# Performance work log

Measured on AMD Instinct MI355X. Metric: run time of the kernel, lower is better.

## Reference

```python
import jax, jax.numpy as jnp
from jax import lax
import numpy as np

D_MODEL = 768
D_STATE = 64
D_CONV = 4
EXPAND = 2
HEADDIM = 128
NGROUPS = 1
D_INNER = EXPAND * D_MODEL            # 1536
NHEADS = D_INNER // HEADDIM           # 12
D_IN_PROJ = 2 * D_INNER + 2 * NGROUPS * D_STATE + NHEADS  # 3212
CONV_DIM = D_INNER + 2 * NGROUPS * D_STATE                # 1664
BATCH, SEQLEN = 2, 4096
EPS = 1e-5


def setup_inputs() -> dict:
    key = jax.random.key(0)
    ks = jax.random.split(key, 8)
    u = jax.random.normal(ks[0], (BATCH, SEQLEN, D_MODEL), jnp.float32)
    W_in = jax.random.normal(ks[1], (D_IN_PROJ, D_MODEL), jnp.float32) * 0.02
    conv_w = jax.random.normal(ks[2], (CONV_DIM, D_CONV), jnp.float32) * 0.2
    conv_b = jnp.zeros((CONV_DIM,), jnp.float32)
    # dt_bias init as in BaseMambaBlock: inv-softplus of dt ~ logU(dt_min, dt_max)
    dt = jnp.exp(jax.random.uniform(ks[3], (NHEADS,)) * (np.log(0.1) - np.log(0.001)) + np.log(0.001))
    dt = jnp.clip(dt, 1e-4, None)
    dt_bias = dt + jnp.log(-jnp.expm1(-dt))
    A_log = jnp.log(jnp.abs(jax.random.normal(ks[4], (NHEADS,), jnp.float32)))
    Dp = jnp.ones((NHEADS,), jnp.float32)
    norm_w = jnp.ones((D_INNER,), jnp.float32)
    W_out = jax.random.normal(ks[5], (D_MODEL, D_INNER), jnp.float32) * 0.02
    return dict(u=u, W_in=W_in, conv_w=conv_w, conv_b=conv_b, dt_bias=dt_bias,
                A_log=A_log, Dp=Dp, norm_w=norm_w, W_out=W_out)


def _silu(x):
    return x * jax.nn.sigmoid(x)


def _depthwise_causal_conv(x, w, b):
    # x: [B, L, C], w: [C, W], b: [C]. Causal: left-pad W-1, crop to L.
    Bt, L, C = x.shape
    xp = jnp.pad(x, ((0, 0), (D_CONV - 1, 0), (0, 0)))
    # stack D_CONV shifted views: [B, L, C, W]
    taps = jnp.stack([xp[:, k:k + L, :] for k in range(D_CONV)], axis=-1)
    return jnp.einsum('blcw,cw->blc', taps, w) + b


def reference(u, W_in, conv_w, conv_b, dt_bias, A_log, Dp, norm_w, W_out):
    Bt, L, _ = u.shape
    zxbcdt = jnp.einsum('bld,ed->ble', u, W_in)  # [B, L, 3212]
    z = zxbcdt[..., :D_INNER]                                   # [B,L,1536]
    xBC = zxbcdt[..., D_INNER:D_INNER + CONV_DIM]               # [B,L,1664]
    dt = zxbcdt[..., D_INNER + CONV_DIM:]                       # [B,L,H]
    dt = jax.nn.softplus(dt + dt_bias)                          # [B,L,H]

    xBC = _silu(_depthwise_causal_conv(xBC, conv_w, conv_b))
    x = xBC[..., :D_INNER].reshape(Bt, L, NHEADS, HEADDIM)      # [B,L,H,P]
    Bm = xBC[..., D_INNER:D_INNER + NGROUPS * D_STATE]          # [B,L,N] (ngroups=1)
    Cm = xBC[..., D_INNER + NGROUPS * D_STATE:]                 # [B,L,N]

    A = -jnp.exp(A_log)                                         # [H]
    dA = jnp.exp(dt * A)                                        # [B,L,H]

    # time-major scan over the selective-state-space recurrence
    xs = (jnp.swapaxes(x, 0, 1),   # [L,B,H,P]
          jnp.swapaxes(dt, 0, 1),  # [L,B,H]
          jnp.swapaxes(dA, 0, 1),  # [L,B,H]
          jnp.swapaxes(Bm, 0, 1),  # [L,B,N]
          jnp.swapaxes(Cm, 0, 1))  # [L,B,N]

    def step(state, inp):
        x_t, dt_t, dA_t, B_t, C_t = inp
        # state: [B,H,P,N]
        state = state * dA_t[..., None, None] + (dt_t[..., None] * x_t)[..., None] * B_t[:, None, None, :]
        y_t = jnp.einsum('bhpn,bn->bhp', state, C_t)
        return state, y_t

    state0 = jnp.zeros((Bt, NHEADS, HEADDIM, D_STATE), u.dtype)
    _, y = lax.scan(step, state0, xs)                           # y: [L,B,H,P]
    y = jnp.swapaxes(y, 0, 1) + Dp[None, None, :, None] * x     # skip term D*x
    y = y.reshape(Bt, L, D_INNER)

    # RMSNormGated, norm_before_gate=False: normalize(y * silu(z)) * weight
    g = y * _silu(z)
    g = g * jax.lax.rsqrt(jnp.mean(g * g, axis=-1, keepdims=True) + EPS) * norm_w
    return jnp.einsum('bli,di->bld', g, W_out)
```

## Files before the change

kernel.cpp:

```cpp
#include <hip/hip_runtime.h>
#include <hip/hip_bf16.h>
#include <stdint.h>

#define BATCH   2
#define SEQLEN  4096
#define DMODEL  768
#define DSTATE  64
#define DCONV   4
#define HEADDIM 128
#define NHEADS  12
#define DINNER  1536
#define DINPROJ 3212
#define CONVDIM 1664
#define DXBC    1676
#define NPAD1   3328
#define ROWS    (BATCH*SEQLEN)
#define CHUNK   64
#define NCHUNK  (SEQLEN/CHUNK)
#define CROWS   8

typedef __bf16 bf16x8 __attribute__((ext_vector_type(8)));
typedef float  f32x4  __attribute__((ext_vector_type(4)));

__device__ __forceinline__ f32x4 splat4(float v) { return (f32x4){v, v, v, v}; }

__device__ __forceinline__ void load_lds16(const void* g, void* l) {
    __builtin_amdgcn_global_load_lds(
        (const __attribute__((address_space(1))) unsigned int*)g,
        (__attribute__((address_space(3))) unsigned int*)l, 16, 0, 0);
}

__global__ void cvt_bf16_kernel(const float* __restrict__ src,
                                __hip_bfloat16* __restrict__ dst, int n) {
    int i = (blockIdx.x * blockDim.x + threadIdx.x) * 4;
    if (i + 3 < n) {
        float4 v = *(const float4*)(src + i);
        dst[i + 0] = __float2bfloat16(v.x);
        dst[i + 1] = __float2bfloat16(v.y);
        dst[i + 2] = __float2bfloat16(v.z);
        dst[i + 3] = __float2bfloat16(v.w);
    } else {
        for (; i < n; ++i) dst[i] = __float2bfloat16(src[i]);
    }
}

__global__ void padw1_kernel(const float* __restrict__ src,
                             __hip_bfloat16* __restrict__ dst) {
    int i = blockIdx.x * blockDim.x + threadIdx.x;
    if (i >= NPAD1 * DMODEL) return;
    int r = i / DMODEL;
    float v = (r < DINPROJ) ? src[i] : 0.f;
    dst[i] = __float2bfloat16(v);
}

__global__ __launch_bounds__(256) void gemm_bf16_nt(
    const __hip_bfloat16* __restrict__ A,
    const __hip_bfloat16* __restrict__ Bt,
    float* __restrict__ C,
    int M, int Nreal, int K, int ldc)
{
    __shared__ __align__(16) __hip_bfloat16 As[128 * 32];
    __shared__ __align__(16) __hip_bfloat16 Bs[128 * 32];
    const int tid  = threadIdx.x;
    const int lane = tid & 63;
    const int wave = tid >> 6;
    const int wm   = wave >> 1;
    const int wn   = wave & 1;
    const int tm   = blockIdx.x * 128;
    const int tn   = blockIdx.y * 128;

    f32x4 acc[4][4] = {};

    const int lrow = tid >> 2;
    const int lk8  = (tid & 3) * 8;
    const __hip_bfloat16* gA0 = A  + (size_t)(tm + lrow)      * K + lk8;
    const __hip_bfloat16* gA1 = A  + (size_t)(tm + lrow + 64) * K + lk8;
    const __hip_bfloat16* gB0 = Bt + (size_t)(tn + lrow)      * K + lk8;
    const __hip_bfloat16* gB1 = Bt + (size_t)(tn + lrow + 64) * K + lk8;
    __hip_bfloat16* sA0 = As + tid * 8;
    __hip_bfloat16* sA1 = As + tid * 8 + 2048;
    __hip_bfloat16* sB0 = Bs + tid * 8;
    __hip_bfloat16* sB1 = Bs + tid * 8 + 2048;

    const int fr = lane & 15;
    const int fk = (lane >> 4) * 8;

    for (int kk = 0; kk < K; kk += 32) {
        load_lds16(gA0 + kk, sA0);
        load_lds16(gA1 + kk, sA1);
        load_lds16(gB0 + kk, sB0);
        load_lds16(gB1 + kk, sB1);
        __syncthreads();
        bf16x8 af[4], bfr[4];
#pragma unroll
        for (int i = 0; i < 4; ++i) {
            af[i]  = *(const bf16x8*)(As + (wm * 64 + i * 16 + fr) * 32 + fk);
            bfr[i] = *(const bf16x8*)(Bs + (wn * 64 + i * 16 + fr) * 32 + fk);
        }
#pragma unroll
        for (int mi = 0; mi < 4; ++mi)
#pragma unroll
            for (int ni = 0; ni < 4; ++ni)
                acc[mi][ni] = __builtin_amdgcn_mfma_f32_16x16x32_bf16(
                    af[mi], bfr[ni], acc[mi][ni], 0, 0, 0);
        __syncthreads();
    }

    const int rq = (lane >> 4) * 4;
#pragma unroll
    for (int mi = 0; mi < 4; ++mi) {
#pragma unroll
        for (int ni = 0; ni < 4; ++ni) {
            int col = tn + wn * 64 + ni * 16 + fr;
            if (col < Nreal) {
                size_t rbase = (size_t)(tm + wm * 64 + mi * 16 + rq) * ldc + col;
#pragma unroll
                for (int j = 0; j < 4; ++j)
                    C[rbase + (size_t)j * ldc] = acc[mi][ni][j];
            }
        }
    }
}

__global__ void conv_kernel(const float* __restrict__ xbcdt,
                            const float* __restrict__ convw,
                            const float* __restrict__ convb,
                            float* __restrict__ xbuf,
                            float* __restrict__ Bm,
                            float* __restrict__ Cm)
{
    int c = blockIdx.x * 256 + threadIdx.x;
    if (c >= CONVDIM) return;
    size_t row0 = (size_t)blockIdx.y * CROWS;
    int l0 = (int)(row0 & (SEQLEN - 1));
    float w0 = convw[c * 4 + 0];
    float w1 = convw[c * 4 + 1];
    float w2 = convw[c * 4 + 2];
    float w3 = convw[c * 4 + 3];
    float bias = convb[c];
    const float* src = xbcdt + row0 * DXBC + c;
    float x0 = (l0 >= 3) ? src[-3 * DXBC] : 0.f;
    float x1 = (l0 >= 2) ? src[-2 * DXBC] : 0.f;
    float x2 = (l0 >= 1) ? src[-1 * DXBC] : 0.f;
#pragma unroll
    for (int r = 0; r < CROWS; ++r) {
        float x3 = src[(size_t)r * DXBC];
        float acc = bias + x0 * w0 + x1 * w1 + x2 * w2 + x3 * w3;
        float v = acc / (1.f + __expf(-acc));
        size_t row = row0 + r;
        if (c < DINNER)               xbuf[row * DINNER + c] = v;
        else if (c < DINNER + DSTATE) Bm[row * DSTATE + (c - DINNER)] = v;
        else                          Cm[row * DSTATE + (c - DINNER - DSTATE)] = v;
        x0 = x1; x1 = x2; x2 = x3;
    }
}

__global__ void dt_kernel(const float* __restrict__ xbcdt,
                          const float* __restrict__ dt_bias,
                          const float* __restrict__ A_log,
                          float* __restrict__ dtb, float* __restrict__ dAb)
{
    int i = blockIdx.x * 256 + threadIdx.x;
    if (i >= ROWS * NHEADS) return;
    int row = i / NHEADS, h = i - row * NHEADS;
    float v = xbcdt[(size_t)row * DXBC + CONVDIM + h] + dt_bias[h];
    float dt = (v > 20.f) ? v : log1pf(__expf(v));
    float A = -__expf(A_log[h]);
    dtb[i] = dt;
    dAb[i] = __expf(dt * A);
}

__global__ __launch_bounds__(256) void chunk_state_f32(
    const float* __restrict__ xbuf, const float* __restrict__ Bm,
    const float* __restrict__ dtb, const float* __restrict__ dAb,
    float* __restrict__ Sloc, float* __restrict__ Pk)
{
    const int blk = blockIdx.x;
    const int k   = blk % NCHUNK;
    const int bh  = blk / NCHUNK;
    const int h   = bh % NHEADS;
    const int b   = bh / NHEADS;
    const int tid = threadIdx.x;
    const int pg  = tid >> 3;
    const int n0  = (tid & 7) * 8;
    const size_t row0 = (size_t)b * SEQLEN + k * CHUNK;
    const float* xbase = xbuf + (row0 * NHEADS + h) * HEADDIM + pg * 4;

    __shared__ __align__(16) float lB[CHUNK][DSTATE];
    __shared__ float lDA[CHUNK];
    __shared__ float ldt[CHUNK];

    for (int i = tid; i < CHUNK * DSTATE / 4; i += 256)
        ((float4*)&lB[0][0])[i] = ((const float4*)(Bm + row0 * DSTATE))[i];
    if (tid < CHUNK) {
        lDA[tid] = dAb[(row0 + tid) * NHEADS + h];
        ldt[tid] = dtb[(row0 + tid) * NHEADS + h];
    }
    __syncthreads();

    f32x4 s4[4][2] = {};
    f32x4 xt0[4], xt1[4];

#pragma unroll
    for (int tt = 0; tt < 4; ++tt)
        xt0[tt] = *(const f32x4*)(xbase + (size_t)tt * (NHEADS * HEADDIM));

#pragma unroll
    for (int tile = 0; tile < 16; ++tile) {
        f32x4* cur = (tile & 1) ? xt1 : xt0;
        f32x4* nxt = (tile & 1) ? xt0 : xt1;
        if (tile < 15) {
#pragma unroll
            for (int tt = 0; tt < 4; ++tt)
                nxt[tt] = *(const f32x4*)(xbase +
                    (size_t)((tile + 1) * 4 + tt) * (NHEADS * HEADDIM));
        }
#pragma unroll
        for (int tt = 0; tt < 4; ++tt) {
            int t = tile * 4 + tt;
            f32x4 da4 = splat4(lDA[t]);
            float dtv = ldt[t];
            f32x4 bv0 = *(const f32x4*)&lB[t][n0];
            f32x4 bv1 = *(const f32x4*)&lB[t][n0 + 4];
#pragma unroll
            for (int pl = 0; pl < 4; ++pl) {
                f32x4 dtx = splat4(dtv * cur[tt][pl]);
                s4[pl][0] = s4[pl][0] * da4 + dtx * bv0;
                s4[pl][1] = s4[pl][1] * da4 + dtx * bv1;
            }
        }
    }

    const size_t kbase = (size_t)(bh * NCHUNK + k) * (HEADDIM * DSTATE);
#pragma unroll
    for (int pl = 0; pl < 4; ++pl) {
        size_t a = kbase + (size_t)(pg * 4 + pl) * DSTATE + n0;
        *(f32x4*)(Sloc + a)     = s4[pl][0];
        *(f32x4*)(Sloc + a + 4) = s4[pl][1];
    }

    if (tid == 0) {
        float pr = 1.f;
#pragma unroll 8
        for (int t = 0; t < CHUNK; ++t) pr *= lDA[t];
        Pk[bh * NCHUNK + k] = pr;
    }
}

__global__ __launch_bounds__(256) void scan_phase2(
    float* __restrict__ Sloc, const float* __restrict__ Pk)
{
    int bh = blockIdx.x >> 5;
    int eo = (blockIdx.x & 31) * 256 + threadIdx.x;
    __shared__ float lP[NCHUNK];
    if (threadIdx.x < NCHUNK) lP[threadIdx.x] = Pk[bh * NCHUNK + threadIdx.x];
    __syncthreads();
    float s = 0.f;
    size_t base = (size_t)bh * NCHUNK * 8192 + eo;
#pragma unroll 8
    for (int k = 0; k < NCHUNK; ++k) {
        size_t a = base + (size_t)k * 8192;
        float f = Sloc[a];
        Sloc[a] = s;
        s = s * lP[k] + f;
    }
}

__global__ __launch_bounds__(256) void chunk_y_f32(
    const float* __restrict__ xbuf, const float* __restrict__ Bm,
    const float* __restrict__ Cm, const float* __restrict__ dtb,
    const float* __restrict__ dAb, const float* __restrict__ Dp,
    const float* __restrict__ Sini, float* __restrict__ ybuf)
{
    const int blk = blockIdx.x;
    const int k   = blk % NCHUNK;
    const int bh  = blk / NCHUNK;
    const int h   = bh % NHEADS;
    const int b   = bh / NHEADS;
    const int tid = threadIdx.x;
    const int pg  = tid >> 2;
    const int q   = tid & 3;
    const int n0  = q * 16;
    const size_t row0 = (size_t)b * SEQLEN + k * CHUNK;
    const float* xbase = xbuf + (row0 * NHEADS + h) * HEADDIM + pg * 2;
    float* ybase = ybuf + (row0 * NHEADS + h) * HEADDIM + pg * 2;

    __shared__ __align__(16) float lB[CHUNK][DSTATE];
    __shared__ __align__(16) float lC[CHUNK][DSTATE];
    __shared__ float lDA[CHUNK];
    __shared__ float ldt[CHUNK];

    for (int i = tid; i < CHUNK * DSTATE / 4; i += 256) {
        ((float4*)&lB[0][0])[i] = ((const float4*)(Bm + row0 * DSTATE))[i];
        ((float4*)&lC[0][0])[i] = ((const float4*)(Cm + row0 * DSTATE))[i];
    }
    if (tid < CHUNK) {
        lDA[tid] = dAb[(row0 + tid) * NHEADS + h];
        ldt[tid] = dtb[(row0 + tid) * NHEADS + h];
    }

    f32x4 s4[2][4];
    const size_t kbase = (size_t)(bh * NCHUNK + k) * (HEADDIM * DSTATE);
#pragma unroll
    for (int pl = 0; pl < 2; ++pl) {
        size_t a = kbase + (size_t)(pg * 2 + pl) * DSTATE + n0;
#pragma unroll
        for (int nq = 0; nq < 4; ++nq)
            s4[pl][nq] = *(const f32x4*)(Sini + a + nq * 4);
    }
    const float dph = Dp[h];

    float xa[2][8], xb[2][8];
#pragma unroll
    for (int tt = 0; tt < 8; ++tt) {
        float2 v = *(const float2*)(xbase + (size_t)tt * (NHEADS * HEADDIM));
        xa[0][tt] = v.x; xa[1][tt] = v.y;
    }
    __syncthreads();

#pragma unroll
    for (int tile = 0; tile < 8; ++tile) {
        float (*cur)[8] = (tile & 1) ? xb : xa;
        float (*nxt)[8] = (tile & 1) ? xa : xb;
        if (tile < 7) {
#pragma unroll
            for (int tt = 0; tt < 8; ++tt) {
                float2 v = *(const float2*)(xbase +
                    (size_t)((tile + 1) * 8 + tt) * (NHEADS * HEADDIM));
                nxt[0][tt] = v.x; nxt[1][tt] = v.y;
            }
        }
#pragma unroll
        for (int tt = 0; tt < 8; ++tt) {
            int t = tile * 8 + tt;
            f32x4 da4 = splat4(lDA[t]);
            float dtv = ldt[t];
            f32x4 bv0 = *(const f32x4*)&lB[t][n0];
            f32x4 bv1 = *(const f32x4*)&lB[t][n0 + 4];
            f32x4 bv2 = *(const f32x4*)&lB[t][n0 + 8];
            f32x4 bv3 = *(const f32x4*)&lB[t][n0 + 12];
            f32x4 cv0 = *(const f32x4*)&lC[t][n0];
            f32x4 cv1 = *(const f32x4*)&lC[t][n0 + 4];
            f32x4 cv2 = *(const f32x4*)&lC[t][n0 + 8];
            f32x4 cv3 = *(const f32x4*)&lC[t][n0 + 12];
            float yr[2];
#pragma unroll
            for (int pl = 0; pl < 2; ++pl) {
                f32x4 dtx = splat4(dtv * cur[pl][tt]);
                f32x4 v0 = s4[pl][0] * da4 + dtx * bv0;
                f32x4 v1 = s4[pl][1] * da4 + dtx * bv1;
                f32x4 v2 = s4[pl][2] * da4 + dtx * bv2;
                f32x4 v3 = s4[pl][3] * da4 + dtx * bv3;
                s4[pl][0] = v0; s4[pl][1] = v1; s4[pl][2] = v2; s4[pl][3] = v3;
                f32x4 y4 = cv0 * v0 + cv1 * v1 + cv2 * v2 + cv3 * v3;
                float y = (y4[0] + y4[1]) + (y4[2] + y4[3]);
                y += __shfl_xor(y, 1);
                y += __shfl_xor(y, 2);
                yr[pl] = y;
            }
            if (q == 0) {
                float2 w = {yr[0] + dph * cur[0][tt], yr[1] + dph * cur[1][tt]};
                *(float2*)(ybase + (size_t)t * (NHEADS * HEADDIM)) = w;
            }
        }
    }
}

#define NT 64
__global__ __launch_bounds__(256) void scan_kernel(
    const float* __restrict__ xbuf, const float* __restrict__ Bm,
    const float* __restrict__ Cm, const float* __restrict__ dtb,
    const float* __restrict__ dAb, const float* __restrict__ Dp,
    float* __restrict__ ybuf)
{
    int blk = blockIdx.x;
    int ps = blk & 7;
    int h  = (blk >> 3) % NHEADS;
    int b  = blk / (NHEADS * 8);
    int p0 = ps * 16;
    int tid = threadIdx.x;
    int pl  = tid >> 4;
    int n0  = (tid & 15) * 4;

    __shared__ __align__(16) float lB[NT][64];
    __shared__ __align__(16) float lC[NT][64];
    __shared__ __align__(16) float lDtx[NT][16];
    __shared__ float lDA[NT];
    __shared__ float lY[NT][16];

    float s0 = 0.f, s1 = 0.f, s2 = 0.f, s3 = 0.f;
    float dph = Dp[h];
    size_t rowbase = (size_t)b * SEQLEN;

    for (int t0 = 0; t0 < SEQLEN; t0 += NT) {
        for (int i = tid; i < NT * 64 / 4; i += 256) {
            ((float4*)&lB[0][0])[i] = ((const float4*)Bm)[(rowbase + t0) * 16 + i];
            ((float4*)&lC[0][0])[i] = ((const float4*)Cm)[(rowbase + t0) * 16 + i];
        }
        for (int i = tid; i < NT * 16; i += 256) {
            int t = i >> 4, pp = i & 15;
            size_t r = rowbase + t0 + t;
            lDtx[t][pp] = dtb[r * NHEADS + h] * xbuf[(r * NHEADS + h) * HEADDIM + p0 + pp];
        }
        if (tid < NT) lDA[tid] = dAb[(rowbase + t0 + tid) * NHEADS + h];
        __syncthreads();

        for (int t = 0; t < NT; ++t) {
            float da  = lDA[t];
            float dtx = lDtx[t][pl];
            const float* bp = &lB[t][n0];
            const float* cp = &lC[t][n0];
            s0 = s0 * da + dtx * bp[0];
            s1 = s1 * da + dtx * bp[1];
            s2 = s2 * da + dtx * bp[2];
            s3 = s3 * da + dtx * bp[3];
            float part = s0 * cp[0] + s1 * cp[1] + s2 * cp[2] + s3 * cp[3];
            part += __shfl_xor(part, 1);
            part += __shfl_xor(part, 2);
            part += __shfl_xor(part, 4);
            part += __shfl_xor(part, 8);
            if ((tid & 15) == 0) lY[t][pl] = part;
        }
        __syncthreads();

        for (int i = tid; i < NT * 16; i += 256) {
            int t = i >> 4, pp = i & 15;
            size_t r = rowbase + t0 + t;
            size_t gi = (r * NHEADS + h) * HEADDIM + p0 + pp;
            ybuf[gi] = lY[t][pp] + dph * xbuf[gi];
        }
        __syncthreads();
    }
}

__global__ __launch_bounds__(256) void gate_rms_kernel(
    const float* __restrict__ ybuf, const float* __restrict__ zbuf,
    const float* __restrict__ norm_w, __hip_bfloat16* __restrict__ gbf)
{
    int row = blockIdx.x;
    int tid = threadIdx.x;
    const float2* y2 = (const float2*)(ybuf + (size_t)row * DINNER);
    const float2* z2 = (const float2*)(zbuf + (size_t)row * DINNER);
    const float2* nw2 = (const float2*)norm_w;
    float g[6];
    float ss = 0.f;
#pragma unroll
    for (int j = 0; j < 3; ++j) {
        int idx = tid + j * 256;
        float2 yy = y2[idx];
        float2 zz = z2[idx];
        float g0 = yy.x * (zz.x / (1.f + __expf(-zz.x)));
        float g1 = yy.y * (zz.y / (1.f + __expf(-zz.y)));
        g[j * 2 + 0] = g0;
        g[j * 2 + 1] = g1;
        ss += g0 * g0 + g1 * g1;
    }
#pragma unroll
    for (int m = 1; m < 64; m <<= 1) ss += __shfl_xor(ss, m);
    __shared__ float red[4];
    if ((tid & 63) == 0) red[tid >> 6] = ss;
    __syncthreads();
    float tot = red[0] + red[1] + red[2] + red[3];
    float scale = rsqrtf(tot * (1.f / DINNER) + 1e-5f);
#pragma unroll
    for (int j = 0; j < 3; ++j) {
        int idx = tid + j * 256;
        float2 w = nw2[idx];
        __hip_bfloat162 o;
        o.x = __float2bfloat16(g[j * 2 + 0] * scale * w.x);
        o.y = __float2bfloat16(g[j * 2 + 1] * scale * w.y);
        *(__hip_bfloat162*)(gbf + (size_t)row * DINNER + idx * 2) = o;
    }
}

extern "C" void kernel_launch(void* const* d_in, const int* in_sizes, int n_in,
                              void* d_out, int out_size, void* d_ws, size_t ws_size,
                              hipStream_t stream)
{
    const float* u       = (const float*)d_in[0];
    const float* W_in    = (const float*)d_in[1];
    const float* conv_w  = (const float*)d_in[2];
    const float* conv_b  = (const float*)d_in[3];
    const float* dt_bias = (const float*)d_in[4];
    const float* A_log   = (const float*)d_in[5];
    const float* Dp      = (const float*)d_in[6];
    const float* norm_w  = (const float*)d_in[7];
    const float* W_out   = (const float*)d_in[8];
    float* out = (float*)d_out;

    char* ws = (char*)d_ws;
    size_t off = 0;
    auto alloc = [&](size_t bytes) {
        char* p = ws + off;
        off += (bytes + 255) & ~(size_t)255;
        return p;
    };
    __hip_bfloat16* ubf  = (__hip_bfloat16*)alloc((size_t)ROWS * DMODEL * 2);
    __hip_bfloat16* W1bf = (__hip_bfloat16*)alloc((size_t)NPAD1 * DMODEL * 2);
    __hip_bfloat16* W2bf = (__hip_bfloat16*)alloc((size_t)DMODEL * DINNER * 2);
    float* zbuf  = (float*)alloc((size_t)ROWS * DINNER * 4);
    float* xbcdt = (float*)alloc((size_t)ROWS * DXBC * 4);
    float* xbuf = (float*)alloc((size_t)ROWS * DINNER * 4);
    float* Bmb  = (float*)alloc((size_t)ROWS * DSTATE * 4);
    float* Cmb  = (float*)alloc((size_t)ROWS * DSTATE * 4);
    float* dtb  = (float*)alloc((size_t)ROWS * NHEADS * 4);
    float* dAb  = (float*)alloc((size_t)ROWS * NHEADS * 4);
    float* ybuf = (float*)alloc((size_t)ROWS * DINNER * 4);
    float* Pkb  = (float*)alloc((size_t)BATCH * NHEADS * NCHUNK * 4);
    __hip_bfloat16* gbf = (__hip_bfloat16*)xbuf;
    float* Sloc = (float*)xbcdt;
    bool chunked = (off <= ws_size);

    cvt_bf16_kernel<<<(ROWS * DMODEL / 4 + 255) / 256, 256, 0, stream>>>(u, ubf, ROWS * DMODEL);
    padw1_kernel<<<(NPAD1 * DMODEL + 255) / 256, 256, 0, stream>>>(W_in, W1bf);
    cvt_bf16_kernel<<<(DMODEL * DINNER / 4 + 255) / 256, 256, 0, stream>>>(W_out, W2bf, DMODEL * DINNER);

    gemm_bf16_nt<<<dim3(ROWS / 128, DINNER / 128), 256, 0, stream>>>(
        ubf, W1bf, zbuf, ROWS, DINNER, DMODEL, DINNER);
    gemm_bf16_nt<<<dim3(ROWS / 128, (DXBC + 127) / 128), 256, 0, stream>>>(
        ubf, W1bf + (size_t)DINNER * DMODEL, xbcdt, ROWS, DXBC, DMODEL, DXBC);

    conv_kernel<<<dim3((CONVDIM + 255) / 256, ROWS / CROWS), 256, 0, stream>>>(
        xbcdt, conv_w, conv_b, xbuf, Bmb, Cmb);

    dt_kernel<<<(ROWS * NHEADS + 255) / 256, 256, 0, stream>>>(xbcdt, dt_bias, A_log, dtb, dAb);

    if (chunked) {
        chunk_state_f32<<<BATCH * NHEADS * NCHUNK, 256, 0, stream>>>(
            xbuf, Bmb, dtb, dAb, Sloc, Pkb);
        scan_phase2<<<BATCH * NHEADS * 32, 256, 0, stream>>>(Sloc, Pkb);
        chunk_y_f32<<<BATCH * NHEADS * NCHUNK, 256, 0, stream>>>(
            xbuf, Bmb, Cmb, dtb, dAb, Dp, Sloc, ybuf);
    } else {
        scan_kernel<<<BATCH * NHEADS * 8, 256, 0, stream>>>(
            xbuf, Bmb, Cmb, dtb, dAb, Dp, ybuf);
    }

    gate_rms_kernel<<<ROWS, 256, 0, stream>>>(ybuf, zbuf, norm_w, gbf);

    gemm_bf16_nt<<<dim3(ROWS / 128, DMODEL / 128), 256, 0, stream>>>(
        gbf, W2bf, out, ROWS, DMODEL, DINNER, DMODEL);
}
```

Baseline: 319.7 us.

## Merge input-projection GEMMs into one launch and widen chunk_y per-thread work

Replaces the two input-projection GEMM launches (z part and xBC/dt part) with a single fused kernel over the padded weight matrix. Each block picks its output buffer from its column-tile index, which removes a launch and the tail imbalance of two separate grids. Separately, chunk_y_f32 now uses 128 threads per block, with each thread owning 4 head-dim rows instead of 2 and loading x as float4. This halves the threads per block and raises register use and per-thread ILP, which may reduce occupancy.

Result: slower. 338.2 us (+5.8%).

```diff
diff --git a/kernel.cpp b/kernel.cpp
--- a/kernel.cpp
+++ b/kernel.cpp
@@ -122,6 +122,81 @@
     }
 }
 
+__global__ __launch_bounds__(256) void gemm1_fused(
+    const __hip_bfloat16* __restrict__ A,
+    const __hip_bfloat16* __restrict__ Bt,
+    float* __restrict__ Cz,
+    float* __restrict__ Cx)
+{
+    __shared__ __align__(16) __hip_bfloat16 As[128 * 32];
+    __shared__ __align__(16) __hip_bfloat16 Bs[128 * 32];
+    const int tid  = threadIdx.x;
+    const int lane = tid & 63;
+    const int wave = tid >> 6;
+    const int wm   = wave >> 1;
+    const int wn   = wave & 1;
+    const int tm   = blockIdx.x * 128;
+    const int tn   = blockIdx.y * 128;
+    const int K    = DMODEL;
+
+    float* Co;
+    int ldc2, cb, nb;
+    if (tn < DINNER) { Co = Cz; ldc2 = DINNER; cb = tn;          nb = DINNER; }
+    else             { Co = Cx; ldc2 = DXBC;   cb = tn - DINNER; nb = DXBC;   }
+
+    f32x4 acc[4][4] = {};
+
+    const int lrow = tid >> 2;
+    const int lk8  = (tid & 3) * 8;
+    const __hip_bfloat16* gA0 = A  + (size_t)(tm + lrow)      * K + lk8;
+    const __hip_bfloat16* gA1 = A  + (size_t)(tm + lrow + 64) * K + lk8;
+    const __hip_bfloat16* gB0 = Bt + (size_t)(tn + lrow)      * K + lk8;
+    const __hip_bfloat16* gB1 = Bt + (size_t)(tn + lrow + 64) * K + lk8;
+    __hip_bfloat16* sA0 = As + tid * 8;
+    __hip_bfloat16* sA1 = As + tid * 8 + 2048;
+    __hip_bfloat16* sB0 = Bs + tid * 8;
+    __hip_bfloat16* sB1 = Bs + tid * 8 + 2048;
+
+    const int fr = lane & 15;
+    const int fk = (lane >> 4) * 8;
+
+    for (int kk = 0; kk < K; kk += 32) {
+        load_lds16(gA0 + kk, sA0);
+        load_lds16(gA1 + kk, sA1);
+        load_lds16(gB0 + kk, sB0);
+        load_lds16(gB1 + kk, sB1);
+        __syncthreads();
+        bf16x8 af[4], bfr[4];
+#pragma unroll
+        for (int i = 0; i < 4; ++i) {
+            af[i]  = *(const bf16x8*)(As + (wm * 64 + i * 16 + fr) * 32 + fk);
+            bfr[i] = *(const bf16x8*)(Bs + (wn * 64 + i * 16 + fr) * 32 + fk);
+        }
+#pragma unroll
+        for (int mi = 0; mi < 4; ++mi)
+#pragma unroll
+            for (int ni = 0; ni < 4; ++ni)
+                acc[mi][ni] = __builtin_amdgcn_mfma_f32_16x16x32_bf16(
+                    af[mi], bfr[ni], acc[mi][ni], 0, 0, 0);
+        __syncthreads();
+    }
+
+    const int rq = (lane >> 4) * 4;
+#pragma unroll
+    for (int mi = 0; mi < 4; ++mi) {
+#pragma unroll
+        for (int ni = 0; ni < 4; ++ni) {
+            int col = cb + wn * 64 + ni * 16 + fr;
+            if (col < nb) {
+                size_t rbase = (size_t)(tm + wm * 64 + mi * 16 + rq) * ldc2 + col;
+#pragma unroll
+                for (int j = 0; j < 4; ++j)
+                    Co[rbase + (size_t)j * ldc2] = acc[mi][ni][j];
+            }
+        }
+    }
+}
+
 __global__ void conv_kernel(const float* __restrict__ xbcdt,
                             const float* __restrict__ convw,
                             const float* __restrict__ convb,
@@ -266,7 +341,7 @@
     }
 }
 
-__global__ __launch_bounds__(256) void chunk_y_f32(
+__global__ __launch_bounds__(128) void chunk_y_f32(
     const float* __restrict__ xbuf, const float* __restrict__ Bm,
     const float* __restrict__ Cm, const float* __restrict__ dtb,
     const float* __restrict__ dAb, const float* __restrict__ Dp,
@@ -282,15 +357,15 @@
     const int q   = tid & 3;
     const int n0  = q * 16;
     const size_t row0 = (size_t)b * SEQLEN + k * CHUNK;
-    const float* xbase = xbuf + (row0 * NHEADS + h) * HEADDIM + pg * 2;
-    float* ybase = ybuf + (row0 * NHEADS + h) * HEADDIM + pg * 2;
+    const float* xbase = xbuf + (row0 * NHEADS + h) * HEADDIM + pg * 4;
+    float* ybase = ybuf + (row0 * NHEADS + h) * HEADDIM + pg * 4;
 
     __shared__ __align__(16) float lB[CHUNK][DSTATE];
     __shared__ __align__(16) float lC[CHUNK][DSTATE];
     __shared__ float lDA[CHUNK];
     __shared__ float ldt[CHUNK];
 
-    for (int i = tid; i < CHUNK * DSTATE / 4; i += 256) {
+    for (int i = tid; i < CHUNK * DSTATE / 4; i += 128) {
         ((float4*)&lB[0][0])[i] = ((const float4*)(Bm + row0 * DSTATE))[i];
         ((float4*)&lC[0][0])[i] = ((const float4*)(Cm + row0 * DSTATE))[i];
     }
@@ -299,40 +374,36 @@
         ldt[tid] = dtb[(row0 + tid) * NHEADS + h];
     }
 
-    f32x4 s4[2][4];
+    f32x4 s4[4][4];
     const size_t kbase = (size_t)(bh * NCHUNK + k) * (HEADDIM * DSTATE);
 #pragma unroll
-    for (int pl = 0; pl < 2; ++pl) {
-        size_t a = kbase + (size_t)(pg * 2 + pl) * DSTATE + n0;
+    for (int pl = 0; pl < 4; ++pl) {
+        size_t a = kbase + (size_t)(pg * 4 + pl) * DSTATE + n0;
 #pragma unroll
         for (int nq = 0; nq < 4; ++nq)
             s4[pl][nq] = *(const f32x4*)(Sini + a + nq * 4);
     }
     const float dph = Dp[h];
 
-    float xa[2][8], xb[2][8];
-#pragma unroll
-    for (int tt = 0; tt < 8; ++tt) {
-        float2 v = *(const float2*)(xbase + (size_t)tt * (NHEADS * HEADDIM));
-        xa[0][tt] = v.x; xa[1][tt] = v.y;
-    }
+    f32x4 xt0[4], xt1[4];
+#pragma unroll
+    for (int tt = 0; tt < 4; ++tt)
+        xt0[tt] = *(const f32x4*)(xbase + (size_t)tt * (NHEADS * HEADDIM));
     __syncthreads();
 
 #pragma unroll
-    for (int tile = 0; tile < 8; ++tile) {
-        float (*cur)[8] = (tile & 1) ? xb : xa;
-        float (*nxt)[8] = (tile & 1) ? xa : xb;
-        if (tile < 7) {
-#pragma unroll
-            for (int tt = 0; tt < 8; ++tt) {
-                float2 v = *(const float2*)(xbase +
-                    (size_t)((tile + 1) * 8 + tt) * (NHEADS * HEADDIM));
-                nxt[0][tt] = v.x; nxt[1][tt] = v.y;
-            }
-        }
-#pragma unroll
-        for (int tt = 0; tt < 8; ++tt) {
-            int t = tile * 8 + tt;
+    for (int tile = 0; tile < 16; ++tile) {
+        f32x4* cur = (tile & 1) ? xt1 : xt0;
+        f32x4* nxt = (tile & 1) ? xt0 : xt1;
+        if (tile < 15) {
+#pragma unroll
+            for (int tt = 0; tt < 4; ++tt)
+                nxt[tt] = *(const f32x4*)(xbase +
+                    (size_t)((tile + 1) * 4 + tt) * (NHEADS * HEADDIM));
+        }
+#pragma unroll
+        for (int tt = 0; tt < 4; ++tt) {
+            int t = tile * 4 + tt;
             f32x4 da4 = splat4(lDA[t]);
             float dtv = ldt[t];
             f32x4 bv0 = *(const f32x4*)&lB[t][n0];
@@ -343,10 +414,10 @@
             f32x4 cv1 = *(const f32x4*)&lC[t][n0 + 4];
             f32x4 cv2 = *(const f32x4*)&lC[t][n0 + 8];
             f32x4 cv3 = *(const f32x4*)&lC[t][n0 + 12];
-            float yr[2];
-#pragma unroll
-            for (int pl = 0; pl < 2; ++pl) {
-                f32x4 dtx = splat4(dtv * cur[pl][tt]);
+            float yr[4];
+#pragma unroll
+            for (int pl = 0; pl < 4; ++pl) {
+                f32x4 dtx = splat4(dtv * cur[tt][pl]);
                 f32x4 v0 = s4[pl][0] * da4 + dtx * bv0;
                 f32x4 v1 = s4[pl][1] * da4 + dtx * bv1;
                 f32x4 v2 = s4[pl][2] * da4 + dtx * bv2;
@@ -359,8 +430,9 @@
                 yr[pl] = y;
             }
             if (q == 0) {
-                float2 w = {yr[0] + dph * cur[0][tt], yr[1] + dph * cur[1][tt]};
-                *(float2*)(ybase + (size_t)t * (NHEADS * HEADDIM)) = w;
+                f32x4 w = {yr[0] + dph * cur[tt][0], yr[1] + dph * cur[tt][1],
+                           yr[2] + dph * cur[tt][2], yr[3] + dph * cur[tt][3]};
+                *(f32x4*)(ybase + (size_t)t * (NHEADS * HEADDIM)) = w;
             }
         }
     }
@@ -515,10 +587,8 @@
     padw1_kernel<<<(NPAD1 * DMODEL + 255) / 256, 256, 0, stream>>>(W_in, W1bf);
     cvt_bf16_kernel<<<(DMODEL * DINNER / 4 + 255) / 256, 256, 0, stream>>>(W_out, W2bf, DMODEL * DINNER);
 
-    gemm_bf16_nt<<<dim3(ROWS / 128, DINNER / 128), 256, 0, stream>>>(
-        ubf, W1bf, zbuf, ROWS, DINNER, DMODEL, DINNER);
-    gemm_bf16_nt<<<dim3(ROWS / 128, (DXBC + 127) / 128), 256, 0, stream>>>(
-        ubf, W1bf + (size_t)DINNER * DMODEL, xbcdt, ROWS, DXBC, DMODEL, DXBC);
+    gemm1_fused<<<dim3(ROWS / 128, NPAD1 / 128), 256, 0, stream>>>(
+        ubf, W1bf, zbuf, xbcdt);
 
     conv_kernel<<<dim3((CONVDIM + 255) / 256, ROWS / CROWS), 256, 0, stream>>>(
         xbcdt, conv_w, conv_b, xbuf, Bmb, Cmb);
@@ -529,7 +599,7 @@
         chunk_state_f32<<<BATCH * NHEADS * NCHUNK, 256, 0, stream>>>(
             xbuf, Bmb, dtb, dAb, Sloc, Pkb);
         scan_phase2<<<BATCH * NHEADS * 32, 256, 0, stream>>>(Sloc, Pkb);
-        chunk_y_f32<<<BATCH * NHEADS * NCHUNK, 256, 0, stream>>>(
+        chunk_y_f32<<<BATCH * NHEADS * NCHUNK, 128, 0, stream>>>(
             xbuf, Bmb, Cmb, dtb, dAb, Dp, Sloc, ybuf);
     } else {
         scan_kernel<<<BATCH * NHEADS * 8, 256, 0, stream>>>(
```
